# Kernel tuning notes

Measured on AMD Instinct MI355X. Metric: run time of the kernel, lower is better.

Reference implementation:

```python
import jax, jax.numpy as jnp
from jax import lax
import numpy as np

B = 128   # per-stream batch (hard-coded via torch.zeros(128, ...))
T = 224   # timesteps
L = 224   # per-timestep signal length
H = 12    # LSTM hidden size


def _conv_chain(x, w1, b1, w2, b2):
    # x: [N, 1, 224] -> [N, 1, 28]
    # Conv1d(k=8, s=4, p=2) -> ReLU -> MaxPool1d(k=4, s=2, p=1) -> ReLU -> Conv1d(k=3, s=1, p=1) -> ReLU
    y = lax.conv_general_dilated(x, w1, (4,), [(2, 2)]) + b1[None, :, None]          # [N,1,56]
    y = jax.nn.relu(y)
    y = lax.reduce_window(y, -jnp.inf, lax.max, (1, 1, 4), (1, 1, 2),
                          [(0, 0), (0, 0), (1, 1)])                                   # [N,1,28]
    y = jax.nn.relu(y)
    y = lax.conv_general_dilated(y, w2, (1,), [(1, 1)]) + b2[None, :, None]          # [N,1,28]
    return jax.nn.relu(y)


def _lstm_bidir(x, Wih, Whh, b):
    # x: [B, T, D]; Wih: [2, 4H, D]; Whh: [2, 4H, H]; b: [2, 4H]; gates in PyTorch order i,f,g,o
    Bn, hid = x.shape[0], Whh.shape[-1]

    def run(xs, wih, whh, bb):
        def step(carry, xt):
            h, c = carry
            g = xt @ wih.T + h @ whh.T + bb
            i, f, gg, o = jnp.split(g, 4, axis=-1)
            c = jax.nn.sigmoid(f) * c + jax.nn.sigmoid(i) * jnp.tanh(gg)
            h = jax.nn.sigmoid(o) * jnp.tanh(c)
            return (h, c), h
        h0 = jnp.zeros((Bn, hid), x.dtype)
        _, ys = lax.scan(step, (h0, h0), xs)
        return ys

    xs = jnp.swapaxes(x, 0, 1)                     # [T, B, D]
    fwd = run(xs, Wih[0], Whh[0], b[0])
    bwd = run(xs[::-1], Whh_fix := Wih[1], Whh[1], b[1])[::-1]
    return jnp.swapaxes(jnp.concatenate([fwd, bwd], axis=-1), 0, 1)  # [B, T, 2H]


def _forward(x, c1w1, c1b1, c1w2, c1b2, c2w1, c2b1, c2w2, c2b2,
             l1_0_Wih, l1_0_Whh, l1_0_b, l1_1_Wih, l1_1_Whh, l1_1_b,
             l2_0_Wih, l2_0_Whh, l2_0_b, l2_1_Wih, l2_1_Whh, l2_1_b,
             fcw1, fcb1, fcw2, fcb2, fcw3, fcb3, w1, w2):
    x1 = x[:B, 0]          # [B, 224, 224]
    x2 = x[B:2 * B, 0]     # [B, 224, 224]
    # Fuse the 224-step Python loop: fold time into the batch of the 1D conv.
    y1 = _conv_chain(x1.reshape(B * T, 1, L), c1w1, c1b1, c1w2, c1b2).reshape(B, T, 28)
    y2 = _conv_chain(x2.reshape(B * T, 1, L), c2w1, c2b1, c2w2, c2b2).reshape(B, T, 28)
    o1 = _lstm_bidir(_lstm_bidir(y1, l1_0_Wih, l1_0_Whh, l1_0_b), l1_1_Wih, l1_1_Whh, l1_1_b)
    o2 = _lstm_bidir(_lstm_bidir(y2, l2_0_Wih, l2_0_Whh, l2_0_b), l2_1_Wih, l2_1_Whh, l2_1_b)
    out = w1 * o1 + w2 * o2                       # [B, T, 24]
    out = out.reshape(B, T * 2 * H)               # [B, 5376]
    out = out @ fcw1.T + fcb1                     # [B, 1024]
    out = out @ fcw2.T + fcb2                     # [B, 192]
    return out @ fcw3.T + fcb3                    # [B, 9]


def setup_inputs():
    key = jax.random.key(0)
    ks = iter(jax.random.split(key, 48))

    def rn(shape, scale=0.1):
        return (scale * jax.random.normal(next(ks), shape)).astype(jnp.float32)

    inp = {"x": rn((2 * B, 1, T, L), 1.0)}
    for s in ("c1", "c2"):
        inp[s + "w1"] = rn((1, 1, 8))
        inp[s + "b1"] = rn((1,))
        inp[s + "w2"] = rn((1, 1, 3))
        inp[s + "b2"] = rn((1,))
    for s in ("l1", "l2"):
        for layer, din in ((0, 28), (1, 2 * H)):
            inp[f"{s}_{layer}_Wih"] = rn((2, 4 * H, din))
            inp[f"{s}_{layer}_Whh"] = rn((2, 4 * H, H))
            inp[f"{s}_{layer}_b"] = rn((2, 4 * H))
    inp["fcw1"] = rn((1024, T * 2 * H), 0.02)
    inp["fcb1"] = rn((1024,))
    inp["fcw2"] = rn((192, 1024), 0.05)
    inp["fcb2"] = rn((192,))
    inp["fcw3"] = rn((9, 192), 0.05)
    inp["fcb3"] = rn((9,))
    inp["w1"] = jnp.ones((1,), jnp.float32)
    inp["w2"] = jnp.ones((1,), jnp.float32)
    return inp


def reference(x, c1w1, c1b1, c1w2, c1b2, c2w1, c2b1, c2w2, c2b2,
              l1_0_Wih, l1_0_Whh, l1_0_b, l1_1_Wih, l1_1_Whh, l1_1_b,
              l2_0_Wih, l2_0_Whh, l2_0_b, l2_1_Wih, l2_1_Whh, l2_1_b,
              fcw1, fcb1, fcw2, fcb2, fcw3, fcb3, w1, w2):
    return _forward(x, c1w1, c1b1, c1w2, c1b2, c2w1, c2b1, c2w2, c2b2,
                    l1_0_Wih, l1_0_Whh, l1_0_b, l1_1_Wih, l1_1_Whh, l1_1_b,
                    l2_0_Wih, l2_0_Whh, l2_0_b, l2_1_Wih, l2_1_Whh, l2_1_b,
                    fcw1, fcb1, fcw2, fcb2, fcw3, fcb3, w1, w2)
```

## Files before the change

### kernel.cpp

```cpp
#include <hip/hip_runtime.h>

#define BB 128
#define TT 224
#define LL 224

typedef float v2f __attribute__((ext_vector_type(2)));

__device__ __forceinline__ float rcpf(float x){ return __builtin_amdgcn_rcpf(x); }

#if __has_builtin(__builtin_amdgcn_exp2f)
#define EXP2(x) __builtin_amdgcn_exp2f(x)
#else
#define EXP2(x) __expf((x)*0.6931471805599453f)
#endif

template<int N>
__device__ __forceinline__ float rorN(float x){
  int xi = __builtin_bit_cast(int, x);
  xi = __builtin_amdgcn_update_dpp(xi, xi, 0x120 + N, 0xf, 0xf, false);
  return __builtin_bit_cast(float, xi);
}

__device__ __forceinline__ void swap32(float& a, float& b){
  asm volatile("s_nop 1\n\tv_permlane32_swap_b32 %0, %1\n\ts_nop 1"
               : "+v"(a), "+v"(b));
}

__global__ __launch_bounds__(256) void convpre_kernel(const float* __restrict__ x,
    const float* __restrict__ c1w1, const float* __restrict__ c1b1,
    const float* __restrict__ c1w2, const float* __restrict__ c1b2,
    const float* __restrict__ c2w1, const float* __restrict__ c2b1,
    const float* __restrict__ c2w2, const float* __restrict__ c2b2,
    const float* __restrict__ l10Wih, const float* __restrict__ l10b,
    const float* __restrict__ l20Wih, const float* __restrict__ l20b,
    float* __restrict__ pre,
    const float* __restrict__ fcw1, const float* __restrict__ fcw2,
    const float* __restrict__ fcw3, const float* __restrict__ fcb1,
    const float* __restrict__ fcb2, const float* __restrict__ fcb3,
    float* __restrict__ wpart, float* __restrict__ BC)
{
  __shared__ float sb[5072];
  int gb  = blockIdx.x;
  int tid = threadIdx.x;

  if (gb < 337){
    if (gb < 336){
      int s = gb / 21, jb = gb % 21;
      for (int i = tid; i < 576; i += 256){
        int o = i >> 6, n = i & 63;
        const float* f3 = fcw3 + o*192;
        const float* f2 = fcw2 + s*64 + n;
        float acc = 0.f;
        for (int p=0;p<192;p++) acc += f3[p]*f2[(size_t)p*1024];
        sb[i] = acc;
      }
      __syncthreads();
      int j = jb*256 + tid;
      float acc[9];
      #pragma unroll
      for (int o=0;o<9;o++) acc[o]=0.f;
      int nbase = s*64;
      #pragma unroll 4
      for (int n=0;n<64;n++){
        float v = fcw1[(size_t)(nbase+n)*5376 + j];
        #pragma unroll
        for (int o=0;o<9;o++) acc[o] += sb[o*64+n]*v;
      }
      #pragma unroll
      for (int o=0;o<9;o++) wpart[((size_t)s*9+o)*5376 + j] = acc[o];
    } else {
      if (tid < 192){
        const float* f2 = fcw2 + (size_t)tid*1024;
        float acc = 0.f;
        for (int n=0;n<1024;n++) acc += f2[n]*fcb1[n];
        sb[tid] = acc;
      }
      __syncthreads();
      if (tid < 9){
        float acc = fcb3[tid];
        const float* f3 = fcw3 + tid*192;
        for (int p=0;p<192;p++) acc += f3[p]*(fcb2[p]+sb[p]);
        BC[tid] = acc;
      }
    }
    return;
  }

  float* xs4  = sb;
  float* c1s  = sb + 3648;
  float* y4   = sb + 4560;

  int blk = gb - 337;
  int branch = (blk >= 1792);
  int lblk = blk - branch*1792;
  int b  = lblk / 14;
  int t0 = (lblk - b*14)*16;
  size_t rbase = ((size_t)(branch*128 + b))*224 + t0;
  size_t prow  = (size_t)b*224 + t0;

  const float* w1 = branch ? c2w1 : c1w1;
  const float* w2 = branch ? c2w2 : c1w2;
  float b1  = branch ? c2b1[0] : c1b1[0];
  float b2v = branch ? c2b2[0] : c1b2[0];
  const float* wih = branch ? l20Wih : l10Wih;
  const float* bia = branch ? l20b   : l10b;

  for (int i = tid; i < 896; i += 256){
    int row = i / 56, c = i - row*56;
    float4 v = *((const float4*)x + (rbase + row)*56 + c);
    int o = row*57 + c;
    xs4[o]          = v.x;
    xs4[912  + o]   = v.y;
    xs4[1824 + o]   = v.z;
    xs4[2736 + o]   = v.w;
  }
  __syncthreads();

  float w1r[8];
  #pragma unroll
  for (int kk=0;kk<8;kk++) w1r[kk]=w1[kk];

  for (int i = tid; i < 896; i += 256){
    int row = i / 56, cj = i - row*56;
    const float* xp = &xs4[row*57 + cj];
    float s = b1;
    if (cj >= 1){
      s += w1r[0]*xp[1824 - 1];
      s += w1r[1]*xp[2736 - 1];
    }
    s += w1r[2]*xp[0];
    s += w1r[3]*xp[912];
    s += w1r[4]*xp[1824];
    s += w1r[5]*xp[2736];
    if (cj <= 54){
      s += w1r[6]*xp[1];
      s += w1r[7]*xp[912 + 1];
    }
    c1s[row*57 + cj] = fmaxf(s, 0.f);
  }
  __syncthreads();

  for (int i = tid; i < 448; i += 256){
    int row = i / 28, j = i - row*28;
    const float* cr = &c1s[row*57];
    float o = b2v;
    #pragma unroll
    for (int pi=0;pi<3;pi++){
      int p = j - 1 + pi;
      float pool = 0.f;
      if (p>=0 && p<28){
        int i0 = 2*p - 1;
        float m = -1e30f;
        #pragma unroll
        for (int q=0;q<4;q++){
          int ii = i0+q;
          if (ii>=0 && ii<56) m = fmaxf(m, cr[ii]);
        }
        pool = fmaxf(m, 0.f);
      }
      o += pool * w2[pi];
    }
    y4[row*32 + j] = fmaxf(o, 0.f);
  }
  __syncthreads();

  if (tid < 192){
    int d   = tid / 96;
    int g96 = tid - d*96;
    int row = g96 % 48;
    int rrg = g96 / 48;
    const float4* wr = (const float4*)(wih + (d*48 + row)*28);
    float4 wv[7];
    #pragma unroll
    for (int q=0;q<7;q++) wv[q] = wr[q];
    float bias = bia[d*48 + row];
    int unit = row % 12, g = row / 12;
    float* prebase = pre + (size_t)(2*branch + d)*(TT*BB*48) + unit*4 + g;
    #pragma unroll
    for (int rq=0; rq<8; rq++){
      int rr = rrg*8 + rq;
      const float4* yv = (const float4*)&y4[rr*32];
      float acc = bias;
      #pragma unroll
      for (int q=0;q<7;q++){
        float4 yq = yv[q];
        acc += yq.x*wv[q].x + yq.y*wv[q].y + yq.z*wv[q].z + yq.w*wv[q].w;
      }
      prebase[(prow + rr)*48] = acc;
    }
  }
}

__global__ __launch_bounds__(256) void pregate2_kernel(
    const float* __restrict__ in,
    const float* __restrict__ wihA, const float* __restrict__ biasA,
    const float* __restrict__ wihB, const float* __restrict__ biasB,
    float* __restrict__ pre,
    const float* __restrict__ wpart, float* __restrict__ Wc)
{
  const int D = 24;
  __shared__ float sb[48*24 + 48];
  int gb  = blockIdx.x;
  int tid = threadIdx.x;

  if (gb < 189){
    int idx = gb*256 + tid;
    float a = 0.f;
    #pragma unroll
    for (int s=0;s<16;s++) a += wpart[(size_t)s*48384 + idx];
    Wc[idx] = a;
    return;
  }

  int pgb = gb - 189;
  float* wL = sb;
  float* bL = sb + 48*D;
  int r = pgb / 1344;
  int lin = (pgb % 1344)*256 + tid;
  int br = r>>1, dir = r&1;
  const float* wih  = (br ? wihB  : wihA)  + dir*48*D;
  const float* bias = (br ? biasB : biasA) + dir*48;
  for (int i = tid; i < 48*D; i += 256) wL[i]=wih[i];
  if (tid < 48) bL[tid]=bias[tid];
  __syncthreads();
  int tb = lin/12;  int k = lin - tb*12;
  const float* rowp = in + (size_t)br*688128 + (size_t)tb*D;
  float aI=bL[k], aF=bL[12+k], aG=bL[24+k], aO=bL[36+k];
  const float4* rp4 = (const float4*)rowp;
  #pragma unroll
  for (int d4=0; d4<D/4; d4++){
    float4 xv = rp4[d4];
    float4 wI = *(const float4*)&wL[(0*12+k)*D + d4*4];
    float4 wF = *(const float4*)&wL[(1*12+k)*D + d4*4];
    float4 wG = *(const float4*)&wL[(2*12+k)*D + d4*4];
    float4 wO = *(const float4*)&wL[(3*12+k)*D + d4*4];
    aI += xv.x*wI.x + xv.y*wI.y + xv.z*wI.z + xv.w*wI.w;
    aF += xv.x*wF.x + xv.y*wF.y + xv.z*wF.z + xv.w*wF.w;
    aG += xv.x*wG.x + xv.y*wG.y + xv.z*wG.z + xv.w*wG.w;
    aO += xv.x*wO.x + xv.y*wO.y + xv.z*wO.z + xv.w*wO.w;
  }
  float4* o = (float4*)(pre + (size_t)r*(TT*BB*48) + (size_t)tb*48 + k*4);
  *o = make_float4(aI,aF,aG,aO);
}

#define LSTM_STEP(P, SS) { \
  float x1=rorN<1>(hv), x2=rorN<2>(hv), x3=rorN<3>(hv), x4=rorN<4>(hv), \
        x5=rorN<5>(hv), x6=rorN<6>(hv), x7=rorN<7>(hv), x8=rorN<8>(hv), \
        x9=rorN<9>(hv), x10=rorN<10>(hv), x11=rorN<11>(hv), x12=rorN<12>(hv), \
        x13=rorN<13>(hv), x14=rorN<14>(hv), x15=rorN<15>(hv); \
  v2f a0 = (P); \
  a0 += w[0]*(v2f){hv,hv};   a0 += w[1]*(v2f){x1,x1};   a0 += w[2]*(v2f){x2,x2};   a0 += w[3]*(v2f){x3,x3}; \
  v2f a1 = w[4]*(v2f){x4,x4};   a1 += w[5]*(v2f){x5,x5};   a1 += w[6]*(v2f){x6,x6};   a1 += w[7]*(v2f){x7,x7}; \
  v2f a2 = w[8]*(v2f){x8,x8};   a2 += w[9]*(v2f){x9,x9};   a2 += w[10]*(v2f){x10,x10}; a2 += w[11]*(v2f){x11,x11}; \
  v2f a3 = w[12]*(v2f){x12,x12}; a3 += w[13]*(v2f){x13,x13}; a3 += w[14]*(v2f){x14,x14}; a3 += w[15]*(v2f){x15,x15}; \
  v2f gg = (a0+a1)+(a2+a3); \
  v2f m  = gg*kmul; \
  v2f e  = { EXP2(m.x), EXP2(m.y) }; \
  e += (v2f){1.f,1.f}; \
  v2f d  = { rcpf(e.x), rcpf(e.y) }; \
  v2f res = ca*d + cb; \
  float p0 = res.x, p1 = res.x; swap32(p0, p1); \
  float q0 = res.y, q1 = res.y; swap32(q0, q1); \
  cst = fmaf(q0, cst, p0*p1); \
  float et = EXP2(cst*2.885390082f); \
  float dt = rcpf(et+1.f); \
  hv = q1*fmaf(-2.f, dt, 1.f); \
  hbuf[SS] = hv; }

#define FLUSH8 { \
  if (doSt){ \
    _Pragma("unroll") \
    for (int q=0;q<8;q++) outP[q*ostep] = hbuf[q]; \
  } \
  outP += 8*ostep; }

__global__ __launch_bounds__(64) __attribute__((amdgpu_waves_per_eu(1,1)))
void lstm_kernel(const float* __restrict__ pre,
    const float* __restrict__ whhA, const float* __restrict__ whhB,
    float* __restrict__ out)
{
  int blk  = blockIdx.x;
  int r    = blk >> 6;
  int br   = r >> 1, dir = r & 1;
  int lane = threadIdx.x;
  int u    = lane & 15;
  int bh   = (lane >> 4) & 1;
  int rbit = lane >> 5;
  int keff = (u < 12) ? u : 11;
  int b    = (blk & 63)*2 + bh;
  const float* whh = (br ? whhB : whhA) + dir*48*12;

  v2f w[16];
  #pragma unroll
  for (int rr=0; rr<16; rr++){
    int j = (u - rr) & 15;
    bool vld = (j < 12) && (u < 12);
    int uw = (u < 12) ? u : 0;
    int jw = (j < 12) ? j : 0;
    float wa = whh[((rbit?24:0)  + uw)*12 + jw];
    float wb = whh[((rbit?36:12) + uw)*12 + jw];
    w[rr] = (v2f){ vld ? wa : 0.f, vld ? wb : 0.f };
  }
  const v2f kmul = rbit ? (v2f){2.885390082f, -1.442695041f}
                        : (v2f){-1.442695041f, -1.442695041f};
  const v2f ca   = rbit ? (v2f){-2.f, 1.f} : (v2f){1.f, 1.f};
  const v2f cb   = rbit ? (v2f){ 1.f, 0.f} : (v2f){0.f, 0.f};

  const float* preR = pre + (size_t)r*(TT*BB*48) + (size_t)b*(TT*48) + keff*4 + rbit*2;
  const int sstep = dir ? -48 : 48;
  int scb = dir ? 223*48 : 0;

  v2f pcur[8], pnext[8];
  #pragma unroll
  for (int i=0;i<8;i++) pcur[i]  = *(const v2f*)(preR + scb +  i   *sstep);
  #pragma unroll
  for (int i=0;i<8;i++) pnext[i] = *(const v2f*)(preR + scb + (i+8)*sstep);
  int lb = scb + 16*sstep;

  float hv = 0.f, cst = 0.f;
  float hbuf[8];
  const int ostep = dir ? -24 : 24;
  float* outP = out + (size_t)br*(BB*TT*24) + (size_t)b*TT*24 + dir*12 + u
              + (size_t)(dir ? 223 : 0)*24;
  const bool doSt = (rbit==0) && (u < 12);

  for (int c=0;c<14;c++){
    LSTM_STEP(pcur[0],0) LSTM_STEP(pcur[1],1) LSTM_STEP(pcur[2],2) LSTM_STEP(pcur[3],3)
    LSTM_STEP(pcur[4],4) LSTM_STEP(pcur[5],5) LSTM_STEP(pcur[6],6) LSTM_STEP(pcur[7],7)
    FLUSH8
    if (c < 13){
      #pragma unroll
      for (int i=0;i<8;i++) pcur[i] = *(const v2f*)(preR + lb + i*sstep);
      lb += 8*sstep;
    }
    LSTM_STEP(pnext[0],0) LSTM_STEP(pnext[1],1) LSTM_STEP(pnext[2],2) LSTM_STEP(pnext[3],3)
    LSTM_STEP(pnext[4],4) LSTM_STEP(pnext[5],5) LSTM_STEP(pnext[6],6) LSTM_STEP(pnext[7],7)
    FLUSH8
    if (c < 13){
      #pragma unroll
      for (int i=0;i<8;i++) pnext[i] = *(const v2f*)(preR + lb + i*sstep);
      lb += 8*sstep;
    }
  }
}

__global__ void final_kernel(const float* __restrict__ o1, const float* __restrict__ o2,
    const float* __restrict__ Wc, const float* __restrict__ BC,
    const float* __restrict__ w1p, const float* __restrict__ w2p,
    float* __restrict__ out)
{
  int wid  = blockIdx.x*4 + (threadIdx.x>>6);
  int lane = threadIdx.x & 63;
  if (wid >= 128*9) return;
  int m = wid / 9, o = wid - m*9;
  float w1 = w1p[0], w2 = w2p[0];
  const float* r1 = o1 + (size_t)m*5376;
  const float* r2 = o2 + (size_t)m*5376;
  const float* wc = Wc + (size_t)o*5376;
  float acc = 0.f;
  for (int i=lane;i<5376;i+=64){
    acc += (w1*r1[i] + w2*r2[i]) * wc[i];
  }
  #pragma unroll
  for (int off=32;off;off>>=1) acc += __shfl_down(acc, off);
  if (lane==0) out[m*9+o] = acc + BC[o];
}

extern "C" void kernel_launch(void* const* d_in, const int* in_sizes, int n_in,
                              void* d_out, int out_size, void* d_ws, size_t ws_size,
                              hipStream_t stream) {
  (void)in_sizes; (void)n_in; (void)out_size; (void)ws_size;
  const float* x    = (const float*)d_in[0];
  const float* c1w1 = (const float*)d_in[1];
  const float* c1b1 = (const float*)d_in[2];
  const float* c1w2 = (const float*)d_in[3];
  const float* c1b2 = (const float*)d_in[4];
  const float* c2w1 = (const float*)d_in[5];
  const float* c2b1 = (const float*)d_in[6];
  const float* c2w2 = (const float*)d_in[7];
  const float* c2b2 = (const float*)d_in[8];
  const float* l10Wih = (const float*)d_in[9];
  const float* l10Whh = (const float*)d_in[10];
  const float* l10b   = (const float*)d_in[11];
  const float* l11Wih = (const float*)d_in[12];
  const float* l11Whh = (const float*)d_in[13];
  const float* l11b   = (const float*)d_in[14];
  const float* l20Wih = (const float*)d_in[15];
  const float* l20Whh = (const float*)d_in[16];
  const float* l20b   = (const float*)d_in[17];
  const float* l21Wih = (const float*)d_in[18];
  const float* l21Whh = (const float*)d_in[19];
  const float* l21b   = (const float*)d_in[20];
  const float* fcw1 = (const float*)d_in[21];
  const float* fcb1 = (const float*)d_in[22];
  const float* fcw2 = (const float*)d_in[23];
  const float* fcb2 = (const float*)d_in[24];
  const float* fcw3 = (const float*)d_in[25];
  const float* fcb3 = (const float*)d_in[26];
  const float* w1   = (const float*)d_in[27];
  const float* w2   = (const float*)d_in[28];
  float* out = (float*)d_out;

  float* ws  = (float*)d_ws;
  float* wpart = ws;
  float* pre  = ws  + 2*802816;
  float* ol0  = pre + 4*1376256;
  float* ol1  = ol0 + 2*688128;
  float* Wc   = ol1 + 2*688128;
  float* BC   = Wc  + 48384;

  convpre_kernel<<<3921,256,0,stream>>>(x, c1w1,c1b1,c1w2,c1b2, c2w1,c2b1,c2w2,c2b2,
      l10Wih, l10b, l20Wih, l20b, pre,
      fcw1, fcw2, fcw3, fcb1, fcb2, fcb3, wpart, BC);
  lstm_kernel<<<256,64,0,stream>>>(pre, l10Whh, l20Whh, ol0);
  pregate2_kernel<<<5565,256,0,stream>>>(ol0, l11Wih, l11b, l21Wih, l21b, pre, wpart, Wc);
  lstm_kernel<<<256,64,0,stream>>>(pre, l11Whh, l21Whh, ol1);
  final_kernel<<<288,256,0,stream>>>(ol1, ol1+688128, Wc, BC, w1, w2, out);
}
```

Baseline: 182.1 us.

## Move FC weight-folding work from conv kernel into idle LSTM kernel blocks

Result: faster. 166.9 us (-8.4%).

```diff
diff --git a/kernel.cpp b/kernel.cpp
--- a/kernel.cpp
+++ b/kernel.cpp
@@ -33,64 +33,17 @@
     const float* __restrict__ c2w2, const float* __restrict__ c2b2,
     const float* __restrict__ l10Wih, const float* __restrict__ l10b,
     const float* __restrict__ l20Wih, const float* __restrict__ l20b,
-    float* __restrict__ pre,
-    const float* __restrict__ fcw1, const float* __restrict__ fcw2,
-    const float* __restrict__ fcw3, const float* __restrict__ fcb1,
-    const float* __restrict__ fcb2, const float* __restrict__ fcb3,
-    float* __restrict__ wpart, float* __restrict__ BC)
+    float* __restrict__ pre)
 {
   __shared__ float sb[5072];
   int gb  = blockIdx.x;
   int tid = threadIdx.x;
 
-  if (gb < 337){
-    if (gb < 336){
-      int s = gb / 21, jb = gb % 21;
-      for (int i = tid; i < 576; i += 256){
-        int o = i >> 6, n = i & 63;
-        const float* f3 = fcw3 + o*192;
-        const float* f2 = fcw2 + s*64 + n;
-        float acc = 0.f;
-        for (int p=0;p<192;p++) acc += f3[p]*f2[(size_t)p*1024];
-        sb[i] = acc;
-      }
-      __syncthreads();
-      int j = jb*256 + tid;
-      float acc[9];
-      #pragma unroll
-      for (int o=0;o<9;o++) acc[o]=0.f;
-      int nbase = s*64;
-      #pragma unroll 4
-      for (int n=0;n<64;n++){
-        float v = fcw1[(size_t)(nbase+n)*5376 + j];
-        #pragma unroll
-        for (int o=0;o<9;o++) acc[o] += sb[o*64+n]*v;
-      }
-      #pragma unroll
-      for (int o=0;o<9;o++) wpart[((size_t)s*9+o)*5376 + j] = acc[o];
-    } else {
-      if (tid < 192){
-        const float* f2 = fcw2 + (size_t)tid*1024;
-        float acc = 0.f;
-        for (int n=0;n<1024;n++) acc += f2[n]*fcb1[n];
-        sb[tid] = acc;
-      }
-      __syncthreads();
-      if (tid < 9){
-        float acc = fcb3[tid];
-        const float* f3 = fcw3 + tid*192;
-        for (int p=0;p<192;p++) acc += f3[p]*(fcb2[p]+sb[p]);
-        BC[tid] = acc;
-      }
-    }
-    return;
-  }
-
   float* xs4  = sb;
   float* c1s  = sb + 3648;
   float* y4   = sb + 4560;
 
-  int blk = gb - 337;
+  int blk = gb;
   int branch = (blk >= 1792);
   int lblk = blk - branch*1792;
   int b  = lblk / 14;
@@ -189,58 +142,6 @@
       prebase[(prow + rr)*48] = acc;
     }
   }
-}
-
-__global__ __launch_bounds__(256) void pregate2_kernel(
-    const float* __restrict__ in,
-    const float* __restrict__ wihA, const float* __restrict__ biasA,
-    const float* __restrict__ wihB, const float* __restrict__ biasB,
-    float* __restrict__ pre,
-    const float* __restrict__ wpart, float* __restrict__ Wc)
-{
-  const int D = 24;
-  __shared__ float sb[48*24 + 48];
-  int gb  = blockIdx.x;
-  int tid = threadIdx.x;
-
-  if (gb < 189){
-    int idx = gb*256 + tid;
-    float a = 0.f;
-    #pragma unroll
-    for (int s=0;s<16;s++) a += wpart[(size_t)s*48384 + idx];
-    Wc[idx] = a;
-    return;
-  }
-
-  int pgb = gb - 189;
-  float* wL = sb;
-  float* bL = sb + 48*D;
-  int r = pgb / 1344;
-  int lin = (pgb % 1344)*256 + tid;
-  int br = r>>1, dir = r&1;
-  const float* wih  = (br ? wihB  : wihA)  + dir*48*D;
-  const float* bias = (br ? biasB : biasA) + dir*48;
-  for (int i = tid; i < 48*D; i += 256) wL[i]=wih[i];
-  if (tid < 48) bL[tid]=bias[tid];
-  __syncthreads();
-  int tb = lin/12;  int k = lin - tb*12;
-  const float* rowp = in + (size_t)br*688128 + (size_t)tb*D;
-  float aI=bL[k], aF=bL[12+k], aG=bL[24+k], aO=bL[36+k];
-  const float4* rp4 = (const float4*)rowp;
-  #pragma unroll
-  for (int d4=0; d4<D/4; d4++){
-    float4 xv = rp4[d4];
-    float4 wI = *(const float4*)&wL[(0*12+k)*D + d4*4];
-    float4 wF = *(const float4*)&wL[(1*12+k)*D + d4*4];
-    float4 wG = *(const float4*)&wL[(2*12+k)*D + d4*4];
-    float4 wO = *(const float4*)&wL[(3*12+k)*D + d4*4];
-    aI += xv.x*wI.x + xv.y*wI.y + xv.z*wI.z + xv.w*wI.w;
-    aF += xv.x*wF.x + xv.y*wF.y + xv.z*wF.z + xv.w*wF.w;
-    aG += xv.x*wG.x + xv.y*wG.y + xv.z*wG.z + xv.w*wG.w;
-    aO += xv.x*wO.x + xv.y*wO.y + xv.z*wO.z + xv.w*wO.w;
-  }
-  float4* o = (float4*)(pre + (size_t)r*(TT*BB*48) + (size_t)tb*48 + k*4);
-  *o = make_float4(aI,aF,aG,aO);
 }
 
 #define LSTM_STEP(P, SS) { \
@@ -277,12 +178,56 @@
 __global__ __launch_bounds__(64) __attribute__((amdgpu_waves_per_eu(1,1)))
 void lstm_kernel(const float* __restrict__ pre,
     const float* __restrict__ whhA, const float* __restrict__ whhB,
-    float* __restrict__ out)
+    float* __restrict__ out,
+    const float* __restrict__ fcw1, const float* __restrict__ fcw2,
+    const float* __restrict__ fcw3, const float* __restrict__ fcb1,
+    float* __restrict__ wpart, float* __restrict__ BCpart)
 {
+  __shared__ float wt[576];
   int blk  = blockIdx.x;
+  int lane = threadIdx.x;
+
+  if (blk >= 256){
+    int xb  = blk - 256;
+    int s   = xb / 84;
+    int j64 = xb % 84;
+    {
+      float acc[9];
+      #pragma unroll
+      for (int q=0;q<9;q++) acc[q]=0.f;
+      const float* f2 = fcw2 + s*64 + lane;
+      for (int p=0;p<192;p++){
+        float v = f2[(size_t)p*1024];
+        #pragma unroll
+        for (int q=0;q<9;q++) acc[q] += fcw3[q*192+p]*v;
+      }
+      #pragma unroll
+      for (int q=0;q<9;q++) wt[q*64+lane] = acc[q];
+    }
+    __syncthreads();
+    int j = j64*64 + lane;
+    float acc[9];
+    #pragma unroll
+    for (int o=0;o<9;o++) acc[o]=0.f;
+    int nbase = s*64;
+    #pragma unroll 4
+    for (int n=0;n<64;n++){
+      float v = fcw1[(size_t)(nbase+n)*5376 + j];
+      #pragma unroll
+      for (int o=0;o<9;o++) acc[o] += wt[o*64+n]*v;
+    }
+    #pragma unroll
+    for (int o=0;o<9;o++) wpart[((size_t)s*9+o)*5376 + j] = acc[o];
+    if (j64 == 0 && lane < 9){
+      float bcp = 0.f;
+      for (int n=0;n<64;n++) bcp += wt[lane*64+n]*fcb1[nbase+n];
+      BCpart[s*9+lane] = bcp;
+    }
+    return;
+  }
+
   int r    = blk >> 6;
   int br   = r >> 1, dir = r & 1;
-  int lane = threadIdx.x;
   int u    = lane & 15;
   int bh   = (lane >> 4) & 1;
   int rbit = lane >> 5;
@@ -342,6 +287,72 @@
       lb += 8*sstep;
     }
   }
+}
+
+__global__ __launch_bounds__(256) void pregate2_kernel(
+    const float* __restrict__ in,
+    const float* __restrict__ wihA, const float* __restrict__ biasA,
+    const float* __restrict__ wihB, const float* __restrict__ biasB,
+    float* __restrict__ pre,
+    const float* __restrict__ wpart, float* __restrict__ Wc,
+    const float* __restrict__ fcw3, const float* __restrict__ fcb2,
+    const float* __restrict__ fcb3, const float* __restrict__ BCpart,
+    float* __restrict__ BC)
+{
+  const int D = 24;
+  __shared__ float sb[48*24 + 48];
+  int gb  = blockIdx.x;
+  int tid = threadIdx.x;
+
+  if (gb < 189){
+    int idx = gb*256 + tid;
+    float a = 0.f;
+    #pragma unroll
+    for (int s=0;s<16;s++) a += wpart[(size_t)s*48384 + idx];
+    Wc[idx] = a;
+    return;
+  }
+  if (gb == 189){
+    if (tid < 9){
+      float acc = fcb3[tid];
+      const float* f3 = fcw3 + tid*192;
+      for (int p=0;p<192;p++) acc += f3[p]*fcb2[p];
+      #pragma unroll
+      for (int s=0;s<16;s++) acc += BCpart[s*9+tid];
+      BC[tid] = acc;
+    }
+    return;
+  }
+
+  int pgb = gb - 190;
+  float* wL = sb;
+  float* bL = sb + 48*D;
+  int r = pgb / 1344;
+  int lin = (pgb % 1344)*256 + tid;
+  int br = r>>1, dir = r&1;
+  const float* wih  = (br ? wihB  : wihA)  + dir*48*D;
+  const float* bias = (br ? biasB : biasA) + dir*48;
+  for (int i = tid; i < 48*D; i += 256) wL[i]=wih[i];
+  if (tid < 48) bL[tid]=bias[tid];
+  __syncthreads();
+  int tb = lin/12;  int k = lin - tb*12;
+  const float* rowp = in + (size_t)br*688128 + (size_t)tb*D;
+  float aI=bL[k], aF=bL[12+k], aG=bL[24+k], aO=bL[36+k];
+  const float4* rp4 = (const float4*)rowp;
+  #pragma unroll
+  for (int d4=0; d4<D/4; d4++){
+    float4 xv = rp4[d4];
+    float4 wI = *(const float4*)&wL[(0*12+k)*D + d4*4];
+    float4 wF = *(const float4*)&wL[(1*12+k)*D + d4*4];
+    float4 wG = *(const float4*)&wL[(2*12+k)*D + d4*4];
+    float4 wO = *(const float4*)&wL[(3*12+k)*D + d4*4];
+    aI += xv.x*wI.x + xv.y*wI.y + xv.z*wI.z + xv.w*wI.w;
+    aF += xv.x*wF.x + xv.y*wF.y + xv.z*wF.z + xv.w*wF.w;
+    aG += xv.x*wG.x + xv.y*wG.y + xv.z*wG.z + xv.w*wG.w;
+    aO += xv.x*wO.x + xv.y*wO.y + xv.z*wO.z + xv.w*wO.w;
+  }
+  float4* o = (float4*)(pre + (size_t)r*(TT*BB*48) + (size_t)tb*48 + k*4);
+  *o = make_float4(aI,aF,aG,aO);
 }
 
 __global__ void final_kernel(const float* __restrict__ o1, const float* __restrict__ o2,
@@ -408,12 +419,15 @@
   float* ol1  = ol0 + 2*688128;
   float* Wc   = ol1 + 2*688128;
   float* BC   = Wc  + 48384;
-
-  convpre_kernel<<<3921,256,0,stream>>>(x, c1w1,c1b1,c1w2,c1b2, c2w1,c2b1,c2w2,c2b2,
-      l10Wih, l10b, l20Wih, l20b, pre,
-      fcw1, fcw2, fcw3, fcb1, fcb2, fcb3, wpart, BC);
-  lstm_kernel<<<256,64,0,stream>>>(pre, l10Whh, l20Whh, ol0);
-  pregate2_kernel<<<5565,256,0,stream>>>(ol0, l11Wih, l11b, l21Wih, l21b, pre, wpart, Wc);
-  lstm_kernel<<<256,64,0,stream>>>(pre, l11Whh, l21Whh, ol1);
+  float* BCpart = BC + 9;
+
+  convpre_kernel<<<3584,256,0,stream>>>(x, c1w1,c1b1,c1w2,c1b2, c2w1,c2b1,c2w2,c2b2,
+      l10Wih, l10b, l20Wih, l20b, pre);
+  lstm_kernel<<<1600,64,0,stream>>>(pre, l10Whh, l20Whh, ol0,
+      fcw1, fcw2, fcw3, fcb1, wpart, BCpart);
+  pregate2_kernel<<<5566,256,0,stream>>>(ol0, l11Wih, l11b, l21Wih, l21b, pre, wpart, Wc,
+      fcw3, fcb2, fcb3, BCpart, BC);
+  lstm_kernel<<<256,64,0,stream>>>(pre, l11Whh, l21Whh, ol1,
+      fcw1, fcw2, fcw3, fcb1, wpart, BCpart);
   final_kernel<<<288,256,0,stream>>>(ol1, ol1+688128, Wc, BC, w1, w2, out);
 }
```
